# Kernel optimization log

Hardware: AMD Instinct MI355X
Metric: run time of the kernel (lower is better)

Reference implementation:

```python
import jax, jax.numpy as jnp
import numpy as np

B, T, D, H = 2, 2048, 1024, 16
DH = D // H
PD = 6
_PAIRS = [(0, 1), (0, 2), (0, 3), (1, 2), (1, 3), (2, 3)]
_J6 = jnp.array([[0, 0, 0, 0, 0, 1], [0, 0, 0, 0, -1, 0], [0, 0, 0, 1, 0, 0],
                 [0, 0, 1, 0, 0, 0], [0, -1, 0, 0, 0, 0], [1, 0, 0, 0, 0, 0]], dtype=jnp.float32)


def exterior(p1, p2):
    # Plucker line coordinates of the 2-plane spanned by p1,p2 in R^4, normalized.
    parts = [p1[..., i] * p2[..., j] - p1[..., j] * p2[..., i] for i, j in _PAIRS]
    L = jnp.stack(parts, axis=-1)
    n = jnp.linalg.norm(L, axis=-1, keepdims=True)
    return L / jnp.maximum(n, 1e-12)


def setup_inputs() -> dict:
    key = jax.random.key(0)
    ks = jax.random.split(key, 12)
    s = 0.02
    A = 0.99 * jnp.broadcast_to(jnp.eye(PD, dtype=jnp.float32), (H, PD, PD))
    return {
        'x': jax.random.normal(ks[0], (B, T, D), jnp.float32),
        'Wqkv': jax.random.normal(ks[1], (D, 3 * D), jnp.float32) * s,
        'bqkv': jnp.zeros((3 * D,), jnp.float32),
        'W1w': jax.random.normal(ks[2], (D, 4 * H), jnp.float32) * s,
        'W2w': jax.random.normal(ks[3], (D, 4 * H), jnp.float32) * s,
        'W1r': jax.random.normal(ks[4], (D, 4 * H), jnp.float32) * s,
        'W2r': jax.random.normal(ks[5], (D, 4 * H), jnp.float32) * s,
        'Wmv': jax.random.normal(ks[6], (D, D), jnp.float32) * s,
        'bmv': jnp.zeros((D,), jnp.float32),
        'Wg': jax.random.normal(ks[7], (D, H), jnp.float32) * s,
        'bg': jnp.zeros((H,), jnp.float32),
        'mem_scale': jnp.full((H,), 0.1, jnp.float32),
        'Wout': jax.random.normal(ks[8], (D, D), jnp.float32) * s,
        'bout': jnp.zeros((D,), jnp.float32),
        'A': A,
    }


def reference(x, Wqkv, bqkv, W1w, W2w, W1r, W2r, Wmv, bmv, Wg, bg, mem_scale, Wout, bout, A):
    Bx, Tx, Dx = x.shape
    # ---- causal softmax attention ----
    qkv = (x @ Wqkv + bqkv).reshape(Bx, Tx, 3, H, DH).transpose(2, 0, 3, 1, 4)
    q, k, v = qkv[0], qkv[1], qkv[2]            # (B,H,T,dh)
    scores = jnp.einsum('bhtd,bhsd->bhts', q, k) * (DH ** -0.5)
    mask = jnp.triu(jnp.ones((Tx, Tx), bool), 1)
    scores = jnp.where(mask, -jnp.inf, scores)
    attn = jax.nn.softmax(scores, axis=-1)      # dropout is identity in eval
    seq_out = jnp.einsum('bhts,bhsd->bthd', attn, v).reshape(Bx, Tx, Dx)
    # ---- write/read lines (Plucker) ----
    x_prev = jnp.concatenate([jnp.zeros((Bx, 1, Dx), x.dtype), x[:, :-1]], axis=1)
    w1 = (x_prev @ W1w).reshape(Bx, Tx, H, 4)
    w2 = (x @ W2w).reshape(Bx, Tx, H, 4)
    write_lines = exterior(w1, w2)              # (B,T,H,6)
    r1 = (x @ W1r).reshape(Bx, Tx, H, 4)
    r2 = (x @ W2r).reshape(Bx, Tx, H, 4)
    read_lines = exterior(r1, r2)               # (B,T,H,6)
    Jw = jnp.einsum('bthi,ij->bthj', write_lines, _J6)
    Jw_T = Jw.transpose(1, 0, 2, 3)             # (T,B,H,6)
    rd_T = read_lines.transpose(1, 0, 2, 3)     # (T,B,H,6)
    # ---- Riccati-style state scan: M_t = A M_{t-1} A^T + Jw_t Jw_t^T ----
    def step(M, ts):
        rd_t, Jw_t = ts                          # (B,H,6)
        score = jnp.einsum('bhp,bhpq,bhq->bh', rd_t, M, rd_t)
        M = jnp.einsum('hpq,bhqr,hsr->bhps', A, M, A) + Jw_t[..., :, None] * Jw_t[..., None, :]
        return M, score
    M0 = jnp.zeros((Bx, H, PD, PD), x.dtype)
    _, scores_T = jax.lax.scan(step, M0, (rd_T, Jw_T))   # (T,B,H)
    mem_score_t = scores_T.transpose(1, 0, 2)            # (B,T,H)
    # ---- gated memory readout ----
    mem_val = x @ Wmv + bmv
    gate = jax.nn.sigmoid(x @ Wg + bg)                   # (B,T,H)
    gated = jax.nn.sigmoid(mem_score_t * mem_scale[None, None, :]) * gate
    gated = gated.mean(axis=-1, keepdims=True)           # (B,T,1)
    return (seq_out + gated * mem_val) @ Wout + bout
```

## Files before the change

### kernel.cpp

```cpp
#include <hip/hip_runtime.h>
#include <cstdint>
#include <cstddef>

typedef unsigned short u16;
typedef unsigned int u32;
typedef __attribute__((ext_vector_type(4))) float f32x4;
typedef __attribute__((ext_vector_type(4))) float float4v;
typedef __attribute__((ext_vector_type(8))) short short8;

#define LDC 4368

__device__ __forceinline__ float bf2f(u16 u){ return __uint_as_float(((u32)u) << 16); }
__device__ __forceinline__ u16 f2bf(float f){
  u32 x = __float_as_uint(f);
  x += 0x7FFFu + ((x >> 16) & 1u);
  return (u16)(x >> 16);
}
__device__ __forceinline__ u16 f2bf_rhu(float f){
  return (u16)((__float_as_uint(f) + 0x8000u) >> 16);
}
#if __has_builtin(__builtin_amdgcn_exp2f)
#define EXP2(x) __builtin_amdgcn_exp2f(x)
#else
#define EXP2(x) exp2f(x)
#endif
__device__ __forceinline__ void mfma16(f32x4& d, short8 a, short8 b){
  d = __builtin_amdgcn_mfma_f32_16x16x32_bf16(a, b, d, 0, 0, 0);
}
__device__ __forceinline__ void async_lds16(void* lds, const void* g){
  __builtin_amdgcn_global_load_lds((const __attribute__((address_space(1))) u32*)g,
                                   (__attribute__((address_space(3))) u32*)lds, 16, 0, 0);
}
__device__ __forceinline__ float sigm(float x){ return 1.f / (1.f + __expf(-x)); }
__device__ __forceinline__ void storev(u16* p, float v){ *p = f2bf(v); }
__device__ __forceinline__ void storev(float* p, float v){ *p = v; }

__device__ __forceinline__ void t32(const float* __restrict__ src, u16* __restrict__ dst,
                                    int R, int Ccols, int c0, int r0, int tid, u16 tile[32][33])
{
  int tx = tid & 31, ty0 = tid >> 5;
  #pragma unroll
  for (int i = 0; i < 4; i++){
    int r = r0 + ty0 + i * 8, c = c0 + tx;
    u16 v = 0;
    if (r < R && c < Ccols) v = f2bf(src[(size_t)r * Ccols + c]);
    tile[ty0 + i * 8][tx] = v;
  }
  __syncthreads();
  #pragma unroll
  for (int i = 0; i < 4; i++){
    int cc = c0 + ty0 + i * 8, rr = r0 + tx;
    if (cc < Ccols && rr < R) dst[(size_t)cc * R + rr] = tile[tx][ty0 + i * 8];
  }
}

__global__ __launch_bounds__(256) void prep_kernel(
    const float* __restrict__ x, const float* __restrict__ bqkv, const float* __restrict__ bmv,
    const float* __restrict__ bg, const float* __restrict__ Wqkv,
    const float* __restrict__ W1w, const float* __restrict__ W2w,
    const float* __restrict__ W1r, const float* __restrict__ W2r,
    const float* __restrict__ Wmv, const float* __restrict__ Wout, const float* __restrict__ Wg,
    u16* __restrict__ xb, float* __restrict__ biasfull, u16* __restrict__ BT, u16* __restrict__ WoutT)
{
  __shared__ u16 tile[32][33];
  const int b = blockIdx.x, tid = threadIdx.x;
  if (b < 2048){
    int i = b * 256 + tid;
    float4v a = *(const float4v*)(x + (size_t)i * 8);
    float4v c = *(const float4v*)(x + (size_t)i * 8 + 4);
    short8 o;
    #pragma unroll
    for (int j = 0; j < 4; j++){ o[j] = (short)f2bf(a[j]); o[4 + j] = (short)f2bf(c[j]); }
    *(short8*)(xb + (size_t)i * 8) = o;
  } else if (b < 2066){
    int i = (b - 2048) * 256 + tid;
    if (i < 4368){
      float v;
      if (i < 3072) v = bqkv[i];
      else if (i < 3328) v = 0.f;
      else if (i < 4352) v = bmv[i - 3328];
      else v = bg[i - 4352];
      biasfull[i] = v;
    }
  } else if (b < 5138){
    int local = b - 2066;
    t32(Wqkv, BT, 1024, 3072, (local % 96) * 32, (local / 96) * 32, tid, tile);
  } else if (b < 5394){
    int local = b - 5138;
    int z = local >> 6, rem = local & 63;
    const float* src = (z == 0) ? W1w : (z == 1) ? W2w : (z == 2) ? W1r : W2r;
    t32(src, BT + (size_t)(3072 + z * 64) * 1024, 1024, 64, (rem & 1) * 32, (rem >> 1) * 32, tid, tile);
  } else if (b < 7442){
    int local = b - 5394;
    int z = local >> 10, rem = local & 1023;
    const float* src = z ? Wout : Wmv;
    u16* dst = z ? WoutT : (BT + (size_t)3328 * 1024);
    t32(src, dst, 1024, 1024, (rem & 31) * 32, (rem >> 5) * 32, tid, tile);
  } else {
    int local = b - 7442;
    t32(Wg, BT + (size_t)4352 * 1024, 1024, 16, 0, local * 32, tid, tile);
  }
}

template<typename OT, int BN>
__global__ __launch_bounds__(256) void gemm_bt(const u16* __restrict__ Ag, const u16* __restrict__ BTg,
                                               const float* __restrict__ bias, OT* __restrict__ Cg,
                                               int M, int N, int K, int ldc)
{
  constexpr int BJ = BN / 64;
  constexpr int NF = BN / 32;
  __shared__ __align__(16) u16 As[2][128 * 32];
  __shared__ __align__(16) u16 Bs[2][BN * 32];
  const int tid = threadIdx.x, lane = tid & 63, w = tid >> 6;
  const int l15 = lane & 15, l4 = lane >> 4;
  const int qx = gridDim.x >> 3, bid = blockIdx.x;
  const int fid = (bid & 7) * qx + (bid >> 3);
  const int m0 = (fid & 31) * 128, n0 = (fid >> 5) * BN;
  const int wr = w >> 1, wc = w & 1;
  f32x4 acc[4][NF] = {};
  const u16* aP[2]; const u16* bP[BJ];
  #pragma unroll
  for (int j = 0; j < 2; j++){
    int i = w * 128 + j * 64 + lane;
    int lrow = i >> 3, cc = i & 7;
    int sc = cc ^ (lrow & 7);
    int grow = lrow * 2 + (sc >> 2);
    int ka = (sc & 3) * 8;
    aP[j] = Ag + (size_t)(m0 + grow) * K + ka;
  }
  #pragma unroll
  for (int j = 0; j < BJ; j++){
    int i = w * (64 * BJ) + j * 64 + lane;
    int lrow = i >> 3, cc = i & 7;
    int sc = cc ^ (lrow & 7);
    int grow = lrow * 2 + (sc >> 2);
    int ka = (sc & 3) * 8;
    int rb = n0 + grow; if (rb > N - 1) rb = N - 1;
    bP[j] = BTg + (size_t)rb * K + ka;
  }
  const int nk = K >> 5;
  #pragma unroll
  for (int j = 0; j < 2; j++)
    async_lds16((char*)As[0] + w * 2048 + j * 1024, aP[j]);
  #pragma unroll
  for (int j = 0; j < BJ; j++)
    async_lds16((char*)Bs[0] + w * (BJ * 1024) + j * 1024, bP[j]);
  __syncthreads();
  for (int t = 0; t < nk; t++){
    const int cur = t & 1;
    if (t + 1 < nk){
      const int k0 = (t + 1) << 5;
      char* An = (char*)As[cur ^ 1] + w * 2048;
      char* Bn = (char*)Bs[cur ^ 1] + w * (BJ * 1024);
      #pragma unroll
      for (int j = 0; j < 2; j++)
        async_lds16(An + j * 1024, aP[j] + k0);
      #pragma unroll
      for (int j = 0; j < BJ; j++)
        async_lds16(Bn + j * 1024, bP[j] + k0);
    }
    const char* Ab = (const char*)As[cur];
    const char* Bb = (const char*)Bs[cur];
    short8 a[4], b[NF];
    #pragma unroll
    for (int mi = 0; mi < 4; mi++){
      int r = wr * 64 + mi * 16 + l15;
      int lrow = r >> 1;
      int slot = (((r & 1) << 2) + l4) ^ (lrow & 7);
      a[mi] = *(const short8*)(Ab + lrow * 128 + slot * 16);
    }
    #pragma unroll
    for (int ni = 0; ni < NF; ni++){
      int r = wc * (BN / 2) + ni * 16 + l15;
      int lrow = r >> 1;
      int slot = (((r & 1) << 2) + l4) ^ (lrow & 7);
      b[ni] = *(const short8*)(Bb + lrow * 128 + slot * 16);
    }
    #pragma unroll
    for (int mi = 0; mi < 4; mi++)
      #pragma unroll
      for (int ni = 0; ni < NF; ni++)
        mfma16(acc[mi][ni], a[mi], b[ni]);
    __syncthreads();
  }
  #pragma unroll
  for (int mi = 0; mi < 4; mi++){
    #pragma unroll
    for (int ni = 0; ni < NF; ni++){
      int col = n0 + wc * (BN / 2) + ni * 16 + l15;
      if (col < N){
        float bv = bias ? bias[col] : 0.f;
        #pragma unroll
        for (int r = 0; r < 4; r++){
          int row = m0 + wr * 64 + mi * 16 + l4 * 4 + r;
          storev(&Cg[(size_t)row * ldc + col], acc[mi][ni][r] + bv);
        }
      }
    }
  }
}

__device__ __forceinline__ void ext6(float* L, const float* p, const float* q){
  L[0] = p[0]*q[1] - p[1]*q[0];
  L[1] = p[0]*q[2] - p[2]*q[0];
  L[2] = p[0]*q[3] - p[3]*q[0];
  L[3] = p[1]*q[2] - p[2]*q[1];
  L[4] = p[1]*q[3] - p[3]*q[1];
  L[5] = p[2]*q[3] - p[3]*q[2];
  float n = sqrtf(L[0]*L[0]+L[1]*L[1]+L[2]*L[2]+L[3]*L[3]+L[4]*L[4]+L[5]*L[5]);
  float inv = 1.f / fmaxf(n, 1e-12f);
  #pragma unroll
  for (int i = 0; i < 6; i++) L[i] *= inv;
}

__global__ __launch_bounds__(256) void chunk_tv_kernel(const u16* __restrict__ C, const float* __restrict__ Ain,
                                                       float* __restrict__ Sb, u16* __restrict__ VT,
                                                       float* __restrict__ rd, float* __restrict__ Jw,
                                                       float* __restrict__ Gk)
{
  __shared__ float Jl[4][384];
  __shared__ float Af[4][36], Ml[4][36], Nl[4][36];
  __shared__ u16 tile[32][33];
  __shared__ float Pw[36], Cur[36];
  const int blk = blockIdx.x, tid = threadIdx.x;
  if (blk < 256){
    const int g = tid >> 6, lt = tid & 63;
    const int task = blk * 4 + g;
    const int c = task & 31, bh = task >> 5, h = bh & 15, b = bh >> 4;
    {
      const int t = c * 64 + lt;
      size_t m = (size_t)b * 2048 + t;
      float w1[4] = {0.f, 0.f, 0.f, 0.f}, w2[4], r1[4], r2[4];
      if (t > 0){
        const u16* p2 = C + (m - 1) * LDC + 3072 + h * 4;
        #pragma unroll
        for (int i = 0; i < 4; i++) w1[i] = bf2f(p2[i]);
      }
      {
        const u16* p2 = C + m * LDC + 3136 + h * 4;
        #pragma unroll
        for (int i = 0; i < 4; i++) w2[i] = bf2f(p2[i]);
        p2 = C + m * LDC + 3200 + h * 4;
        #pragma unroll
        for (int i = 0; i < 4; i++) r1[i] = bf2f(p2[i]);
        p2 = C + m * LDC + 3264 + h * 4;
        #pragma unroll
        for (int i = 0; i < 4; i++) r2[i] = bf2f(p2[i]);
      }
      float L[6], R[6];
      ext6(L, w1, w2);
      ext6(R, r1, r2);
      size_t o = ((size_t)bh * 2048 + t) * 6;
      #pragma unroll
      for (int i = 0; i < 6; i++) rd[o + i] = R[i];
      float jv[6] = { L[5], -L[4], L[3], L[2], -L[1], L[0] };
      #pragma unroll
      for (int i = 0; i < 6; i++){ Jw[o + i] = jv[i]; Jl[g][lt * 6 + i] = jv[i]; }
    }
    const int p = lt / 6, q = lt % 6;
    if (lt < 36){ Af[g][lt] = Ain[h * 36 + lt]; Ml[g][lt] = 0.f; }
    __syncthreads();
    float arow[6], acol[6];
    if (lt < 36){
      #pragma unroll
      for (int k = 0; k < 6; k++){ arow[k] = Af[g][p * 6 + k]; acol[k] = Af[g][q * 6 + k]; }
    }
    for (int s = 0; s < 64; s++){
      float n = 0.f;
      if (lt < 36){
        #pragma unroll
        for (int k = 0; k < 6; k++) n += arow[k] * Ml[g][k * 6 + q];
        Nl[g][lt] = n;
      }
      __syncthreads();
      if (lt < 36){
        float m = Jl[g][s * 6 + p] * Jl[g][s * 6 + q];
        #pragma unroll
        for (int k = 0; k < 6; k++) m += Nl[g][p * 6 + k] * acol[k];
        Ml[g][lt] = m;
      }
      __syncthreads();
    }
    if (lt < 36) Sb[((size_t)bh * 32 + c) * 36 + lt] = Ml[g][lt];
  } else if (blk < 272){
    const int h = blk - 256;
    const int p = tid / 6, q = tid % 6;
    if (tid < 36){
      Pw[tid] = Ain[h * 36 + tid];
      float id = (p == q) ? 1.f : 0.f;
      Cur[tid] = id;
      Gk[(size_t)h * 65 * 36 + tid] = id;
    }
    __syncthreads();
    for (int k = 1; k <= 64; k++){
      float v = 0.f;
      if (tid < 36){
        #pragma unroll
        for (int j = 0; j < 6; j++) v += Cur[p * 6 + j] * Pw[j * 6 + q];
      }
      __syncthreads();
      if (tid < 36){
        Cur[tid] = v;
        Gk[((size_t)h * 65 + k) * 36 + tid] = v;
      }
      __syncthreads();
    }
  } else {
    int local = blk - 272;
    int bh = local >> 7, rem = local & 127;
    int b = bh >> 4, h = bh & 15;
    const u16* src = C + (size_t)b * 2048 * LDC + 2048 + h * 64;
    int c0 = (rem & 1) * 32, r0 = (rem >> 1) * 32;
    int tx = tid & 31, ty0 = tid >> 5;
    #pragma unroll
    for (int i = 0; i < 4; i++)
      tile[ty0 + i * 8][tx] = src[(size_t)(r0 + ty0 + i * 8) * LDC + c0 + tx];
    __syncthreads();
    u16* dstb = VT + (size_t)bh * 64 * 2048;
    #pragma unroll
    for (int i = 0; i < 4; i++)
      dstb[(size_t)(c0 + ty0 + i * 8) * 2048 + r0 + tx] = tile[tx][ty0 + i * 8];
  }
}

__global__ __launch_bounds__(256) void attn_score_kernel(const u16* __restrict__ C, const u16* __restrict__ VT,
                                                         u16* __restrict__ seqb,
                                                         const float* __restrict__ rd, const float* __restrict__ Jw,
                                                         const float* __restrict__ Gk, const float* __restrict__ Sb,
                                                         float* __restrict__ score)
{
  __shared__ __align__(16) char smem[40960];
  const int blk = blockIdx.x, tid = threadIdx.x;
  if (blk >= 256){
    char* KsB = smem;
    char* VsB = smem + 16384;
    const int abk = blk - 256;
    const int bh = abk & 31, bb = bh >> 4, h = bh & 15;
    const int qblk = 31 - (abk >> 5);
    const int lane = tid & 63, w = tid >> 6;
    const int l15 = lane & 15, l4 = lane >> 4;
    u16* Psw = (u16*)(smem + 32768) + w * 1024;
    const int q0 = qblk * 64 + w * 16;
    const float csc = 0.1803368801f;
    const u16* qb = C + (size_t)(bb * 2048 + q0 + l15) * LDC + h * 64 + l4 * 8;
    short8 qf0 = *(const short8*)qb;
    short8 qf1 = *(const short8*)(qb + 32);
    #pragma unroll
    for (int j = 0; j < 8; j++){
      qf0[j] = (short)f2bf(bf2f((u16)qf0[j]) * csc);
      qf1[j] = (short)f2bf(bf2f((u16)qf1[j]) * csc);
    }
    f32x4 o[4] = {};
    float mrun[4], lsum[4];
    #pragma unroll
    for (int r = 0; r < 4; r++){ mrun[r] = -1e30f; lsum[r] = 0.f; }
    const int nkv = qblk + 1;
    const int rowA = tid >> 3, chA = tid & 7;
    const int swA = chA ^ (rowA & 7);
    const u16* Kg = C + (size_t)(bb * 2048) * LDC + 1024 + h * 64 + chA * 8;
    const u16* Vg = VT + ((size_t)bh * 64 + rowA) * 2048 + chA * 8;
    short8 kr0, kr1, vr0, vr1;
    kr0 = *(const short8*)(Kg + (size_t)rowA * LDC);
    kr1 = *(const short8*)(Kg + (size_t)(rowA + 32) * LDC);
    vr0 = *(const short8*)(Vg);
    vr1 = *(const short8*)(Vg + 32 * 2048);
    *(short8*)(KsB + rowA * 128 + swA * 16)        = kr0;
    *(short8*)(KsB + (rowA + 32) * 128 + swA * 16) = kr1;
    *(short8*)(VsB + rowA * 128 + swA * 16)        = vr0;
    *(short8*)(VsB + (rowA + 32) * 128 + swA * 16) = vr1;
    if (nkv > 1){
      kr0 = *(const short8*)(Kg + (size_t)(64 + rowA) * LDC);
      kr1 = *(const short8*)(Kg + (size_t)(64 + rowA + 32) * LDC);
      vr0 = *(const short8*)(Vg + 64);
      vr1 = *(const short8*)(Vg + 64 + 32 * 2048);
    }
    for (int i = 0; i < nkv; i++){
      const int cur = i & 1;
      __syncthreads();
      if (i + 1 < nkv){
        char* Kd = KsB + (cur ^ 1) * 8192;
        char* Vd = VsB + (cur ^ 1) * 8192;
        *(short8*)(Kd + rowA * 128 + swA * 16)        = kr0;
        *(short8*)(Kd + (rowA + 32) * 128 + swA * 16) = kr1;
        *(short8*)(Vd + rowA * 128 + swA * 16)        = vr0;
        *(short8*)(Vd + (rowA + 32) * 128 + swA * 16) = vr1;
        if (i + 2 < nkv){
          int nx = (i + 2) * 64;
          kr0 = *(const short8*)(Kg + (size_t)(nx + rowA) * LDC);
          kr1 = *(const short8*)(Kg + (size_t)(nx + rowA + 32) * LDC);
          vr0 = *(const short8*)(Vg + nx);
          vr1 = *(const short8*)(Vg + nx + 32 * 2048);
        }
      }
      const char* Ks = KsB + cur * 8192;
      const char* Vs = VsB + cur * 8192;
      const bool diag = (i == qblk);
      f32x4 s4[4] = {};
      __builtin_amdgcn_s_setprio(1);
      #pragma unroll
      for (int j = 0; j < 4; j++){
        const int srow = j * 16 + l15, rm = srow & 7;
        const char* base = Ks + srow * 128;
        short8 b0 = *(const short8*)(base + ((l4 ^ rm) << 4));
        short8 b1 = *(const short8*)(base + (((4 + l4) ^ rm) << 4));
        mfma16(s4[j], qf0, b0);
        mfma16(s4[j], qf1, b1);
      }
      __builtin_amdgcn_s_setprio(0);
      float ps[4][4], lm[4];
      #pragma unroll
      for (int r = 0; r < 4; r++){
        float v0 = s4[0][r], v1 = s4[1][r], v2 = s4[2][r], v3 = s4[3][r];
        if (diag){
          int qrow = w * 16 + l4 * 4 + r;
          if (l15 > qrow)      v0 = -1e30f;
          if (16 + l15 > qrow) v1 = -1e30f;
          if (32 + l15 > qrow) v2 = -1e30f;
          if (48 + l15 > qrow) v3 = -1e30f;
        }
        lm[r] = fmaxf(fmaxf(v0, v1), fmaxf(v2, v3));
        ps[r][0] = v0; ps[r][1] = v1; ps[r][2] = v2; ps[r][3] = v3;
      }
      int ok = (lm[0] <= mrun[0] + 11.5f) && (lm[1] <= mrun[1] + 11.5f)
            && (lm[2] <= mrun[2] + 11.5f) && (lm[3] <= mrun[3] + 11.5f);
      if (!__all(ok)){
        #pragma unroll
        for (int r = 0; r < 4; r++){
          float mx = lm[r];
          mx = fmaxf(mx, __shfl_xor(mx, 1));
          mx = fmaxf(mx, __shfl_xor(mx, 2));
          mx = fmaxf(mx, __shfl_xor(mx, 4));
          mx = fmaxf(mx, __shfl_xor(mx, 8));
          float mnew = fmaxf(mrun[r], mx);
          float sc = EXP2(mrun[r] - mnew);
          mrun[r] = mnew;
          lsum[r] *= sc;
          o[0][r] *= sc; o[1][r] *= sc; o[2][r] *= sc; o[3][r] *= sc;
        }
      }
      #pragma unroll
      for (int r = 0; r < 4; r++){
        float p0 = EXP2(ps[r][0] - mrun[r]);
        float p1 = EXP2(ps[r][1] - mrun[r]);
        float p2 = EXP2(ps[r][2] - mrun[r]);
        float p3 = EXP2(ps[r][3] - mrun[r]);
        lsum[r] += (p0 + p1) + (p2 + p3);
        ps[r][0] = p0; ps[r][1] = p1; ps[r][2] = p2; ps[r][3] = p3;
      }
      char* pw = (char*)Psw;
      const int cb = (l15 & 7) * 2;
      #pragma unroll
      for (int r = 0; r < 4; r++){
        const int prow = l4 * 4 + r, rm = prow & 7;
        char* prb = pw + prow * 128 + cb;
        #pragma unroll
        for (int j = 0; j < 4; j++){
          int cj = (j * 2 + (l15 >> 3)) ^ rm;
          *((u16*)(prb + cj * 16)) = f2bf_rhu(ps[r][j]);
        }
      }
      const int prm = l15 & 7;
      short8 pa0 = *(const short8*)(pw + l15 * 128 + ((l4 ^ prm) << 4));
      short8 pa1 = *(const short8*)(pw + l15 * 128 + (((4 + l4) ^ prm) << 4));
      __builtin_amdgcn_s_setprio(1);
      #pragma unroll
      for (int j = 0; j < 4; j++){
        const int drow = j * 16 + l15, rm = drow & 7;
        const char* vb = Vs + drow * 128;
        short8 b0 = *(const short8*)(vb + ((l4 ^ rm) << 4));
        short8 b1 = *(const short8*)(vb + (((4 + l4) ^ rm) << 4));
        mfma16(o[j], pa0, b0);
        mfma16(o[j], pa1, b1);
      }
      __builtin_amdgcn_s_setprio(0);
    }
    #pragma unroll
    for (int r = 0; r < 4; r++){
      float ls = lsum[r];
      ls += __shfl_xor(ls, 1);
      ls += __shfl_xor(ls, 2);
      ls += __shfl_xor(ls, 4);
      ls += __shfl_xor(ls, 8);
      float inv = 1.f / ls;
      size_t base = (size_t)(bb * 2048 + q0 + l4 * 4 + r) * 1024 + h * 64;
      seqb[base + l15]      = f2bf(o[0][r] * inv);
      seqb[base + 16 + l15] = f2bf(o[1][r] * inv);
      seqb[base + 32 + l15] = f2bf(o[2][r] * inv);
      seqb[base + 48 + l15] = f2bf(o[3][r] * inv);
    }
  } else {
    float* Gl  = (float*)smem;
    float* Jl  = (float*)(smem + 9216);
    float* Bl  = (float*)(smem + 16896);
    float* A64s= (float*)(smem + 17472);
    float* Bw  = (float*)(smem + 17664);
    float* Nw  = (float*)(smem + 17856);
    const int local = blk;
    const int tblk = local & 7, bh = local >> 3, h = bh & 15;
    const int t0 = tblk * 256;
    for (int i = tid; i < 64 * 36; i += 256) Gl[i] = Gk[(size_t)h * 65 * 36 + i];
    {
      int base = t0 * 6 - 384;
      for (int i = tid; i < 1920; i += 256){
        int s6 = base + i;
        Jl[i] = (s6 >= 0) ? Jw[(size_t)bh * (2048 * 6) + s6] : 0.f;
      }
    }
    {
      const int p = tid / 6, q = tid % 6;
      if (tid < 36){ A64s[tid] = Gk[((size_t)h * 65 + 64) * 36 + tid]; Bw[tid] = 0.f; }
      __syncthreads();
      float arow[6], acol[6];
      if (tid < 36){
        #pragma unroll
        for (int k = 0; k < 6; k++){ arow[k] = A64s[p * 6 + k]; acol[k] = A64s[q * 6 + k]; }
      }
      const int cEnd = tblk * 4;
      for (int c = 0; c < cEnd + 4; c++){
        if (tid < 36 && c >= cEnd) Bl[(c - cEnd) * 36 + tid] = Bw[tid];
        float n = 0.f;
        if (tid < 36){
          #pragma unroll
          for (int k = 0; k < 6; k++) n += arow[k] * Bw[k * 6 + q];
        }
        __syncthreads();
        if (tid < 36) Nw[tid] = n;
        __syncthreads();
        if (tid < 36){
          float m = Sb[((size_t)bh * 32 + c) * 36 + tid];
          #pragma unroll
          for (int k = 0; k < 6; k++) m += Nw[p * 6 + k] * acol[k];
          Bw[tid] = m;
        }
        __syncthreads();
      }
    }
    __syncthreads();
    float Ar[36];
    #pragma unroll
    for (int i = 0; i < 36; i++) Ar[i] = Gl[36 + i];
    const int t = t0 + tid;
    const int cl = tid >> 6;
    const int dlt = tid & 63;
    float rdv[6];
    {
      const float* rp = rd + ((size_t)bh * 2048 + t) * 6;
      #pragma unroll
      for (int q = 0; q < 6; q++) rdv[q] = rp[q];
    }
    const float* g = Gl + dlt * 36;
    float u[6];
    #pragma unroll
    for (int p = 0; p < 6; p++){
      float s = 0.f;
      #pragma unroll
      for (int q = 0; q < 6; q++) s += rdv[q] * g[q * 6 + p];
      u[p] = s;
    }
    float acc = 0.f;
    #pragma unroll
    for (int p = 0; p < 6; p++){
      float bv = 0.f;
      #pragma unroll
      for (int q = 0; q < 6; q++) bv += Bl[cl * 36 + p * 6 + q] * u[q];
      acc += u[p] * bv;
    }
    float wv[6];
    #pragma unroll
    for (int q = 0; q < 6; q++) wv[q] = rdv[q];
    const int sIdx = tid + 63;
    for (int k = 0; k < dlt; k++){
      const float* jp = Jl + (sIdx - k) * 6;
      float uu = wv[0]*jp[0] + wv[1]*jp[1] + wv[2]*jp[2] + wv[3]*jp[3] + wv[4]*jp[4] + wv[5]*jp[5];
      acc += uu * uu;
      float nw[6];
      #pragma unroll
      for (int q = 0; q < 6; q++)
        nw[q] = wv[0]*Ar[q] + wv[1]*Ar[6+q] + wv[2]*Ar[12+q] + wv[3]*Ar[18+q] + wv[4]*Ar[24+q] + wv[5]*Ar[30+q];
      #pragma unroll
      for (int q = 0; q < 6; q++) wv[q] = nw[q];
    }
    score[(size_t)bh * 2048 + t] = acc;
  }
}

__global__ __launch_bounds__(256) void gated_combine_kernel(const float* __restrict__ score, const u16* __restrict__ C,
                                                            const float* __restrict__ mem_scale,
                                                            const u16* __restrict__ seqb, u16* __restrict__ preb)
{
  __shared__ float gsh[2];
  const int blk = blockIdx.x, tid = threadIdx.x;
  const int m0 = blk * 2;
  if (tid < 32){
    const int mm = tid >> 4, h2 = tid & 15;
    const int m = m0 + mm;
    const int b = m >> 11, t = m & 2047;
    float sc = score[(size_t)(b * 16 + h2) * 2048 + t];
    float v = sigm(sc * mem_scale[h2]) * sigm(bf2f(C[(size_t)m * LDC + 4352 + h2]));
    v += __shfl_xor(v, 1);
    v += __shfl_xor(v, 2);
    v += __shfl_xor(v, 4);
    v += __shfl_xor(v, 8);
    if (h2 == 0) gsh[mm] = v * (1.f / 16.f);
  }
  __syncthreads();
  const int m = m0 + (tid >> 7), d8 = (tid & 127) * 8;
  const float g = gsh[tid >> 7];
  short8 sv = *(const short8*)(seqb + (size_t)m * 1024 + d8);
  short8 mv = *(const short8*)(C + (size_t)m * LDC + 3328 + d8);
  short8 ov;
  #pragma unroll
  for (int j = 0; j < 8; j++){
    float f = bf2f((u16)sv[j]) + g * bf2f((u16)mv[j]);
    ov[j] = (short)f2bf(f);
  }
  *(short8*)(preb + (size_t)m * 1024 + d8) = ov;
}

extern "C" void kernel_launch(void* const* d_in, const int* in_sizes, int n_in,
                              void* d_out, int out_size, void* d_ws, size_t ws_size,
                              hipStream_t stream)
{
  (void)in_sizes; (void)n_in; (void)out_size; (void)ws_size;
  const float* x     = (const float*)d_in[0];
  const float* Wqkv  = (const float*)d_in[1];
  const float* bqkv  = (const float*)d_in[2];
  const float* W1w   = (const float*)d_in[3];
  const float* W2w   = (const float*)d_in[4];
  const float* W1r   = (const float*)d_in[5];
  const float* W2r   = (const float*)d_in[6];
  const float* Wmv   = (const float*)d_in[7];
  const float* bmv   = (const float*)d_in[8];
  const float* Wg    = (const float*)d_in[9];
  const float* bg    = (const float*)d_in[10];
  const float* mem_scale = (const float*)d_in[11];
  const float* Wout  = (const float*)d_in[12];
  const float* bout  = (const float*)d_in[13];
  const float* Am    = (const float*)d_in[14];
  float* out = (float*)d_out;

  char* p = (char*)d_ws;
  auto carve = [&](size_t bytes) -> void* {
    void* r = (void*)p;
    p += (bytes + 255) & ~(size_t)255;
    return r;
  };
  u16*   xb       = (u16*)  carve((size_t)4096 * 1024 * 2);
  u16*   C        = (u16*)  carve((size_t)4096 * LDC * 2);
  u16*   BT       = (u16*)  carve((size_t)LDC * 1024 * 2);
  u16*   WoutT    = (u16*)  carve((size_t)1024 * 1024 * 2);
  float* biasfull = (float*)carve((size_t)LDC * 4);
  u16*   VTb      = (u16*)  carve((size_t)32 * 64 * 2048 * 2);
  u16*   seqb     = (u16*)  carve((size_t)4096 * 1024 * 2);
  float* rdb      = (float*)carve((size_t)32 * 2048 * 6 * 4);
  float* Jwb      = (float*)carve((size_t)32 * 2048 * 6 * 4);
  float* Gk       = (float*)carve((size_t)16 * 65 * 36 * 4);
  float* Sbb      = (float*)carve((size_t)32 * 32 * 36 * 4);
  float* scoreb   = (float*)carve((size_t)32 * 2048 * 4);
  u16*   preb     = (u16*)  carve((size_t)4096 * 1024 * 2);

  prep_kernel<<<7474, 256, 0, stream>>>(x, bqkv, bmv, bg, Wqkv, W1w, W2w, W1r, W2r,
                                        Wmv, Wout, Wg, xb, biasfull, BT, WoutT);

  gemm_bt<u16, 128><<<1120, 256, 0, stream>>>(xb, BT, biasfull, C, 4096, LDC, 1024, LDC);

  chunk_tv_kernel<<<4368, 256, 0, stream>>>(C, Am, Sbb, VTb, rdb, Jwb, Gk);

  attn_score_kernel<<<1280, 256, 0, stream>>>(C, VTb, seqb, rdb, Jwb, Gk, Sbb, scoreb);

  gated_combine_kernel<<<2048, 256, 0, stream>>>(scoreb, C, mem_scale, seqb, preb);

  gemm_bt<float, 64><<<512, 256, 0, stream>>>(preb, WoutT, bout, out, 4096, 1024, 1024, 1024);
}
```

Before: 165.0 us.

## Pair heavy and light causal query blocks per workgroup to balance attention work

Each attention workgroup now processes two query blocks, hi and 31-hi, sharing the same streamed K/V tiles, so every block does a near-equal amount of causal work. The attention grid shrinks from 1024 to 512 blocks, and the K/V loaded into shared memory is reused for both query tiles. This removes the tail imbalance of triangular causal work and halves K/V traffic for the light tile. The cost is higher register pressure from two sets of accumulators and Q fragments, which may lower occupancy.

```diff
diff --git a/kernel.cpp b/kernel.cpp
--- a/kernel.cpp
+++ b/kernel.cpp
@@ -336,29 +336,124 @@
     char* VsB = smem + 16384;
     const int abk = blk - 256;
     const int bh = abk & 31, bb = bh >> 4, h = bh & 15;
-    const int qblk = 31 - (abk >> 5);
+    const int hi = 31 - (abk >> 4 >> 1);
+    const int lo = 31 - hi;
     const int lane = tid & 63, w = tid >> 6;
     const int l15 = lane & 15, l4 = lane >> 4;
     u16* Psw = (u16*)(smem + 32768) + w * 1024;
-    const int q0 = qblk * 64 + w * 16;
     const float csc = 0.1803368801f;
-    const u16* qb = C + (size_t)(bb * 2048 + q0 + l15) * LDC + h * 64 + l4 * 8;
-    short8 qf0 = *(const short8*)qb;
-    short8 qf1 = *(const short8*)(qb + 32);
+    const int q0h = hi * 64 + w * 16, q0l = lo * 64 + w * 16;
+    short8 qh0, qh1, ql0, ql1;
+    {
+      const u16* qb = C + (size_t)(bb * 2048 + q0h + l15) * LDC + h * 64 + l4 * 8;
+      qh0 = *(const short8*)qb;
+      qh1 = *(const short8*)(qb + 32);
+      const u16* qb2 = C + (size_t)(bb * 2048 + q0l + l15) * LDC + h * 64 + l4 * 8;
+      ql0 = *(const short8*)qb2;
+      ql1 = *(const short8*)(qb2 + 32);
+    }
     #pragma unroll
     for (int j = 0; j < 8; j++){
-      qf0[j] = (short)f2bf(bf2f((u16)qf0[j]) * csc);
-      qf1[j] = (short)f2bf(bf2f((u16)qf1[j]) * csc);
-    }
-    f32x4 o[4] = {};
-    float mrun[4], lsum[4];
-    #pragma unroll
-    for (int r = 0; r < 4; r++){ mrun[r] = -1e30f; lsum[r] = 0.f; }
-    const int nkv = qblk + 1;
+      qh0[j] = (short)f2bf(bf2f((u16)qh0[j]) * csc);
+      qh1[j] = (short)f2bf(bf2f((u16)qh1[j]) * csc);
+      ql0[j] = (short)f2bf(bf2f((u16)ql0[j]) * csc);
+      ql1[j] = (short)f2bf(bf2f((u16)ql1[j]) * csc);
+    }
+    f32x4 oh[4] = {}, ol[4] = {};
+    float mrunh[4], lsumh[4], mrunl[4], lsuml[4];
+    #pragma unroll
+    for (int r = 0; r < 4; r++){
+      mrunh[r] = -1e30f; lsumh[r] = 0.f;
+      mrunl[r] = -1e30f; lsuml[r] = 0.f;
+    }
+    const int nkv = hi + 1;
     const int rowA = tid >> 3, chA = tid & 7;
     const int swA = chA ^ (rowA & 7);
     const u16* Kg = C + (size_t)(bb * 2048) * LDC + 1024 + h * 64 + chA * 8;
     const u16* Vg = VT + ((size_t)bh * 64 + rowA) * 2048 + chA * 8;
+
+    auto compute = [&](const char* Ks, const char* Vs, short8 qa0, short8 qa1,
+                       f32x4 (&o)[4], float (&mrun)[4], float (&lsum)[4], bool diag){
+      f32x4 s4[4] = {};
+      __builtin_amdgcn_s_setprio(1);
+      #pragma unroll
+      for (int j = 0; j < 4; j++){
+        const int srow = j * 16 + l15, rm = srow & 7;
+        const char* base = Ks + srow * 128;
+        short8 b0 = *(const short8*)(base + ((l4 ^ rm) << 4));
+        short8 b1 = *(const short8*)(base + (((4 + l4) ^ rm) << 4));
+        mfma16(s4[j], qa0, b0);
+        mfma16(s4[j], qa1, b1);
+      }
+      __builtin_amdgcn_s_setprio(0);
+      float ps[4][4], lm[4];
+      #pragma unroll
+      for (int r = 0; r < 4; r++){
+        float v0 = s4[0][r], v1 = s4[1][r], v2 = s4[2][r], v3 = s4[3][r];
+        if (diag){
+          int qrow = w * 16 + l4 * 4 + r;
+          if (l15 > qrow)      v0 = -1e30f;
+          if (16 + l15 > qrow) v1 = -1e30f;
+          if (32 + l15 > qrow) v2 = -1e30f;
+          if (48 + l15 > qrow) v3 = -1e30f;
+        }
+        lm[r] = fmaxf(fmaxf(v0, v1), fmaxf(v2, v3));
+        ps[r][0] = v0; ps[r][1] = v1; ps[r][2] = v2; ps[r][3] = v3;
+      }
+      int ok = (lm[0] <= mrun[0] + 11.5f) && (lm[1] <= mrun[1] + 11.5f)
+            && (lm[2] <= mrun[2] + 11.5f) && (lm[3] <= mrun[3] + 11.5f);
+      if (!__all(ok)){
+        #pragma unroll
+        for (int r = 0; r < 4; r++){
+          float mx = lm[r];
+          mx = fmaxf(mx, __shfl_xor(mx, 1));
+          mx = fmaxf(mx, __shfl_xor(mx, 2));
+          mx = fmaxf(mx, __shfl_xor(mx, 4));
+          mx = fmaxf(mx, __shfl_xor(mx, 8));
+          float mnew = fmaxf(mrun[r], mx);
+          float sc = EXP2(mrun[r] - mnew);
+          mrun[r] = mnew;
+          lsum[r] *= sc;
+          o[0][r] *= sc; o[1][r] *= sc; o[2][r] *= sc; o[3][r] *= sc;
+        }
+      }
+      #pragma unroll
+      for (int r = 0; r < 4; r++){
+        float p0 = EXP2(ps[r][0] - mrun[r]);
+        float p1 = EXP2(ps[r][1] - mrun[r]);
+        float p2 = EXP2(ps[r][2] - mrun[r]);
+        float p3 = EXP2(ps[r][3] - mrun[r]);
+        lsum[r] += (p0 + p1) + (p2 + p3);
+        ps[r][0] = p0; ps[r][1] = p1; ps[r][2] = p2; ps[r][3] = p3;
+      }
+      char* pw = (char*)Psw;
+      const int cb = (l15 & 7) * 2;
+      #pragma unroll
+      for (int r = 0; r < 4; r++){
+        const int prow = l4 * 4 + r, rm = prow & 7;
+        char* prb = pw + prow * 128 + cb;
+        #pragma unroll
+        for (int j = 0; j < 4; j++){
+          int cj = (j * 2 + (l15 >> 3)) ^ rm;
+          *((u16*)(prb + cj * 16)) = f2bf_rhu(ps[r][j]);
+        }
+      }
+      const int prm = l15 & 7;
+      short8 pa0 = *(const short8*)(pw + l15 * 128 + ((l4 ^ prm) << 4));
+      short8 pa1 = *(const short8*)(pw + l15 * 128 + (((4 + l4) ^ prm) << 4));
+      __builtin_amdgcn_s_setprio(1);
+      #pragma unroll
+      for (int j = 0; j < 4; j++){
+        const int drow = j * 16 + l15, rm = drow & 7;
+        const char* vb = Vs + drow * 128;
+        short8 b0 = *(const short8*)(vb + ((l4 ^ rm) << 4));
+        short8 b1 = *(const short8*)(vb + (((4 + l4) ^ rm) << 4));
+        mfma16(o[j], pa0, b0);
+        mfma16(o[j], pa1, b1);
+      }
+      __builtin_amdgcn_s_setprio(0);
+    };
+
     short8 kr0, kr1, vr0, vr1;
     kr0 = *(const short8*)(Kg + (size_t)rowA * LDC);
     kr1 = *(const short8*)(Kg + (size_t)(rowA + 32) * LDC);
@@ -394,99 +489,36 @@
       }
       const char* Ks = KsB + cur * 8192;
       const char* Vs = VsB + cur * 8192;
-      const bool diag = (i == qblk);
-      f32x4 s4[4] = {};
-      __builtin_amdgcn_s_setprio(1);
-      #pragma unroll
-      for (int j = 0; j < 4; j++){
-        const int srow = j * 16 + l15, rm = srow & 7;
-        const char* base = Ks + srow * 128;
-        short8 b0 = *(const short8*)(base + ((l4 ^ rm) << 4));
-        short8 b1 = *(const short8*)(base + (((4 + l4) ^ rm) << 4));
-        mfma16(s4[j], qf0, b0);
-        mfma16(s4[j], qf1, b1);
-      }
-      __builtin_amdgcn_s_setprio(0);
-      float ps[4][4], lm[4];
-      #pragma unroll
-      for (int r = 0; r < 4; r++){
-        float v0 = s4[0][r], v1 = s4[1][r], v2 = s4[2][r], v3 = s4[3][r];
-        if (diag){
-          int qrow = w * 16 + l4 * 4 + r;
-          if (l15 > qrow)      v0 = -1e30f;
-          if (16 + l15 > qrow) v1 = -1e30f;
-          if (32 + l15 > qrow) v2 = -1e30f;
-          if (48 + l15 > qrow) v3 = -1e30f;
-        }
-        lm[r] = fmaxf(fmaxf(v0, v1), fmaxf(v2, v3));
-        ps[r][0] = v0; ps[r][1] = v1; ps[r][2] = v2; ps[r][3] = v3;
-      }
-      int ok = (lm[0] <= mrun[0] + 11.5f) && (lm[1] <= mrun[1] + 11.5f)
-            && (lm[2] <= mrun[2] + 11.5f) && (lm[3] <= mrun[3] + 11.5f);
-      if (!__all(ok)){
-        #pragma unroll
-        for (int r = 0; r < 4; r++){
-          float mx = lm[r];
-          mx = fmaxf(mx, __shfl_xor(mx, 1));
-          mx = fmaxf(mx, __shfl_xor(mx, 2));
-          mx = fmaxf(mx, __shfl_xor(mx, 4));
-          mx = fmaxf(mx, __shfl_xor(mx, 8));
-          float mnew = fmaxf(mrun[r], mx);
-          float sc = EXP2(mrun[r] - mnew);
-          mrun[r] = mnew;
-          lsum[r] *= sc;
-          o[0][r] *= sc; o[1][r] *= sc; o[2][r] *= sc; o[3][r] *= sc;
-        }
-      }
-      #pragma unroll
-      for (int r = 0; r < 4; r++){
-        float p0 = EXP2(ps[r][0] - mrun[r]);
-        float p1 = EXP2(ps[r][1] - mrun[r]);
-        float p2 = EXP2(ps[r][2] - mrun[r]);
-        float p3 = EXP2(ps[r][3] - mrun[r]);
-        lsum[r] += (p0 + p1) + (p2 + p3);
-        ps[r][0] = p0; ps[r][1] = p1; ps[r][2] = p2; ps[r][3] = p3;
-      }
-      char* pw = (char*)Psw;
-      const int cb = (l15 & 7) * 2;
-      #pragma unroll
-      for (int r = 0; r < 4; r++){
-        const int prow = l4 * 4 + r, rm = prow & 7;
-        char* prb = pw + prow * 128 + cb;
-        #pragma unroll
-        for (int j = 0; j < 4; j++){
-          int cj = (j * 2 + (l15 >> 3)) ^ rm;
-          *((u16*)(prb + cj * 16)) = f2bf_rhu(ps[r][j]);
-        }
-      }
-      const int prm = l15 & 7;
-      short8 pa0 = *(const short8*)(pw + l15 * 128 + ((l4 ^ prm) << 4));
-      short8 pa1 = *(const short8*)(pw + l15 * 128 + (((4 + l4) ^ prm) << 4));
-      __builtin_amdgcn_s_setprio(1);
-      #pragma unroll
-      for (int j = 0; j < 4; j++){
-        const int drow = j * 16 + l15, rm = drow & 7;
-        const char* vb = Vs + drow * 128;
-        short8 b0 = *(const short8*)(vb + ((l4 ^ rm) << 4));
-        short8 b1 = *(const short8*)(vb + (((4 + l4) ^ rm) << 4));
-        mfma16(o[j], pa0, b0);
-        mfma16(o[j], pa1, b1);
-      }
-      __builtin_amdgcn_s_setprio(0);
+      compute(Ks, Vs, qh0, qh1, oh, mrunh, lsumh, i == hi);
+      if (i <= lo) compute(Ks, Vs, ql0, ql1, ol, mrunl, lsuml, i == lo);
     }
     #pragma unroll
     for (int r = 0; r < 4; r++){
-      float ls = lsum[r];
+      float ls = lsumh[r];
       ls += __shfl_xor(ls, 1);
       ls += __shfl_xor(ls, 2);
       ls += __shfl_xor(ls, 4);
       ls += __shfl_xor(ls, 8);
       float inv = 1.f / ls;
-      size_t base = (size_t)(bb * 2048 + q0 + l4 * 4 + r) * 1024 + h * 64;
-      seqb[base + l15]      = f2bf(o[0][r] * inv);
-      seqb[base + 16 + l15] = f2bf(o[1][r] * inv);
-      seqb[base + 32 + l15] = f2bf(o[2][r] * inv);
-      seqb[base + 48 + l15] = f2bf(o[3][r] * inv);
+      size_t base = (size_t)(bb * 2048 + q0h + l4 * 4 + r) * 1024 + h * 64;
+      seqb[base + l15]      = f2bf(oh[0][r] * inv);
+      seqb[base + 16 + l15] = f2bf(oh[1][r] * inv);
+      seqb[base + 32 + l15] = f2bf(oh[2][r] * inv);
+      seqb[base + 48 + l15] = f2bf(oh[3][r] * inv);
+    }
+    #pragma unroll
+    for (int r = 0; r < 4; r++){
+      float ls = lsuml[r];
+      ls += __shfl_xor(ls, 1);
+      ls += __shfl_xor(ls, 2);
+      ls += __shfl_xor(ls, 4);
+      ls += __shfl_xor(ls, 8);
+      float inv = 1.f / ls;
+      size_t base = (size_t)(bb * 2048 + q0l + l4 * 4 + r) * 1024 + h * 64;
+      seqb[base + l15]      = f2bf(ol[0][r] * inv);
+      seqb[base + 16 + l15] = f2bf(ol[1][r] * inv);
+      seqb[base + 32 + l15] = f2bf(ol[2][r] * inv);
+      seqb[base + 48 + l15] = f2bf(ol[3][r] * inv);
     }
   } else {
     float* Gl  = (float*)smem;
@@ -666,7 +698,7 @@
 
   chunk_tv_kernel<<<4368, 256, 0, stream>>>(C, Am, Sbb, VTb, rdb, Jwb, Gk);
 
-  attn_score_kernel<<<1280, 256, 0, stream>>>(C, VTb, seqb, rdb, Jwb, Gk, Sbb, scoreb);
+  attn_score_kernel<<<768, 256, 0, stream>>>(C, VTb, seqb, rdb, Jwb, Gk, Sbb, scoreb);
 
   gated_combine_kernel<<<2048, 256, 0, stream>>>(scoreb, C, mem_scale, seqb, preb);
 
```

New measurement: 177.4 us. +7.5%, slower.
